# Performance work log

Measured on AMD Instinct MI355X. Metric: run time of the kernel, lower is better.

## Reference

```python
import jax, jax.numpy as jnp
import numpy as np

ALPHA = 0.2  # leaky relu negative slope
NEG_INF = -9e15


def setup_inputs() -> dict:
    key = jax.random.key(0)
    k1, k2, k3, k4, k5 = jax.random.split(key, 5)
    N, F_in, F_out, E = 4096, 64, 64, 8
    x = jax.random.normal(k1, (N, F_in), dtype=jnp.float32)
    adj = jax.random.randint(k2, (N, N), 0, 2, dtype=jnp.int32)
    edge_feats = jax.random.normal(k3, (N, N, E), dtype=jnp.float32)
    W = jax.random.normal(k4, (F_in, F_out), dtype=jnp.float32) * 0.1
    a = jax.random.normal(k5, (2 * F_out + E, 1), dtype=jnp.float32) * 0.1
    return {"x": x, "adj": adj, "edge_feats": edge_feats, "W": W, "a": a}


def reference(x, adj, edge_feats, W, a):
    F_out = W.shape[1]
    h = x @ W  # [N, F_out]
    # Original builds a_input[i,j] = concat(h_i, h_j, ef_ij) and dots with a.
    # Equivalent decomposition: e[i,j] = h_i.a1 + h_j.a2 + ef_ij.a3
    a1 = a[:F_out, 0]            # [F_out]
    a2 = a[F_out:2 * F_out, 0]   # [F_out]
    a3 = a[2 * F_out:, 0]        # [E]
    s1 = h @ a1                  # [N]
    s2 = h @ a2                  # [N]
    s3 = jnp.einsum('ije,e->ij', edge_feats, a3)  # [N, N]
    e = s1[:, None] + s2[None, :] + s3
    e = jnp.where(e > 0, e, ALPHA * e)  # leaky relu
    scores = jnp.where(adj > 0, e, NEG_INF)
    attention = jax.nn.softmax(scores, axis=1)
    # dropout p=0.0 (eval) -> identity
    h_prime = attention @ h  # [N, F_out]
    return jax.nn.elu(h_prime)  # concat=True
```

## Files before the change

kernel.cpp:

```cpp
#include <hip/hip_runtime.h>
#include <cstdint>
#include <cstddef>

#define LRELU_ALPHA 0.2f


typedef float f4 __attribute__((ext_vector_type(4)));

__device__ __forceinline__ f4 nt4(const float* p) {
    return __builtin_nontemporal_load((const f4*)p);
}

__global__ __launch_bounds__(256) void gat_prep(
    const float* __restrict__ x, const float* __restrict__ W,
    const float* __restrict__ a, float* __restrict__ h,
    float* __restrict__ s1, float* __restrict__ s2)
{
    __shared__ float Wl[64 * 64];
    const int tid = threadIdx.x;
    for (int idx = tid; idx < 64 * 64; idx += 256) Wl[idx] = W[idx];
    __syncthreads();

    const int wave = tid >> 6;
    const int lane = tid & 63;
    const int i = blockIdx.x * 4 + wave;

    const float xv = x[i * 64 + lane];
    float hv = 0.f;
#pragma unroll
    for (int k = 0; k < 64; ++k)
        hv = fmaf(__shfl(xv, k), Wl[k * 64 + lane], hv);
    h[i * 64 + lane] = hv;

    float v1 = hv * a[lane];
    float v2 = hv * a[64 + lane];
#pragma unroll
    for (int off = 32; off >= 1; off >>= 1) {
        v1 += __shfl_xor(v1, off);
        v2 += __shfl_xor(v2, off);
    }
    if (lane == 0) { s1[i] = v1; s2[i] = v2; }
}

__device__ __forceinline__ float bcast(float v, int l) {
    return __int_as_float(__builtin_amdgcn_readlane(__float_as_int(v), l));
}

__global__ __launch_bounds__(256, 4) void gat_attn(
    const float* __restrict__ ef, const int* __restrict__ adj,
    const float* __restrict__ a, const float* __restrict__ h,
    const float* __restrict__ s1, const float* __restrict__ s2,
    float* __restrict__ out)
{
    __shared__ float accs[4][4][64];
    __shared__ float lsums[4][4];

    const int tid  = threadIdx.x;
    const int w    = tid >> 6;
    const int lane = tid & 63;
    const int i0   = blockIdx.x * 4;

    float a3[8];
#pragma unroll
    for (int e = 0; e < 8; ++e) a3[e] = a[128 + e];

    float s1r[4];
#pragma unroll
    for (int r = 0; r < 4; ++r) s1r[r] = s1[i0 + r];

    float acc0 = 0.f, acc1 = 0.f, acc2 = 0.f, acc3 = 0.f;
    float ls0 = 0.f, ls1 = 0.f, ls2 = 0.f, ls3 = 0.f;

    const size_t efrow = (size_t)4096 * 8;

    int ad[4];
#pragma unroll
    for (int r = 0; r < 4; ++r)
        ad[r] = __builtin_nontemporal_load(adj + (size_t)(i0 + r) * 4096 + tid);

    for (int k = 0; k < 16; ++k) {
        const int j = tid + (k << 8);
        const float s2j = s2[j];

        int adn[4];
        if (k < 15) {
#pragma unroll
            for (int r = 0; r < 4; ++r)
                adn[r] = __builtin_nontemporal_load(
                    adj + (size_t)(i0 + r) * 4096 + j + 256);
        }

        float p0, p1, p2, p3;
        {
            float pv[4];
#pragma unroll
            for (int r = 0; r < 4; ++r) {
                float p = 0.f;
                if (ad[r] > 0) {
                    const float* efp = ef + (size_t)(i0 + r) * efrow + (size_t)j * 8;
                    const f4 e0 = nt4(efp);
                    const f4 e1 = nt4(efp + 4);
                    float s3 = e0.x * a3[0] + e0.y * a3[1] + e0.z * a3[2] + e0.w * a3[3]
                             + e1.x * a3[4] + e1.y * a3[5] + e1.z * a3[6] + e1.w * a3[7];
                    float e = s1r[r] + s2j + s3;
                    e = (e > 0.f) ? e : LRELU_ALPHA * e;
                    p = __expf(e);
                }
                pv[r] = p;
            }
            p0 = pv[0]; p1 = pv[1]; p2 = pv[2]; p3 = pv[3];
        }
        ls0 += p0; ls1 += p1; ls2 += p2; ls3 += p3;

        const int jw0 = (w << 6) + (k << 8);
        const float* __restrict__ hp = h + (size_t)jw0 * 64 + lane;
#pragma unroll 8
        for (int l = 0; l < 64; ++l) {
            const float hv = hp[l * 64];
            acc0 = fmaf(bcast(p0, l), hv, acc0);
            acc1 = fmaf(bcast(p1, l), hv, acc1);
            acc2 = fmaf(bcast(p2, l), hv, acc2);
            acc3 = fmaf(bcast(p3, l), hv, acc3);
        }

#pragma unroll
        for (int r = 0; r < 4; ++r) ad[r] = adn[r];
    }

#pragma unroll
    for (int off = 32; off >= 1; off >>= 1) {
        ls0 += __shfl_xor(ls0, off);
        ls1 += __shfl_xor(ls1, off);
        ls2 += __shfl_xor(ls2, off);
        ls3 += __shfl_xor(ls3, off);
    }
    if (lane == 0) {
        lsums[w][0] = ls0; lsums[w][1] = ls1;
        lsums[w][2] = ls2; lsums[w][3] = ls3;
    }
    accs[w][0][lane] = acc0;
    accs[w][1][lane] = acc1;
    accs[w][2][lane] = acc2;
    accs[w][3][lane] = acc3;
    __syncthreads();

    const float v = accs[0][w][lane] + accs[1][w][lane]
                  + accs[2][w][lane] + accs[3][w][lane];
    const float S = lsums[0][w] + lsums[1][w] + lsums[2][w] + lsums[3][w];
    float o = v / S;
    o = (o > 0.f) ? o : (__expf(o) - 1.f);
    out[(size_t)(i0 + w) * 64 + lane] = o;
}

extern "C" void kernel_launch(void* const* d_in, const int* in_sizes, int n_in,
                              void* d_out, int out_size, void* d_ws, size_t ws_size,
                              hipStream_t stream) {
    const float* x   = (const float*)d_in[0];
    const int*   adj = (const int*)  d_in[1];
    const float* ef  = (const float*)d_in[2];
    const float* W   = (const float*)d_in[3];
    const float* a   = (const float*)d_in[4];
    float* out = (float*)d_out;

    float* h  = (float*)d_ws;
    float* s1 = h + 4096 * 64;
    float* s2 = s1 + 4096;

    gat_prep<<<1024, 256, 0, stream>>>(x, W, a, h, s1, s2);
    gat_attn<<<1024, 256, 0, stream>>>(ef, adj, a, h, s1, s2, out);
}
```

Measured before the change: 759.7 us.

## Software-pipeline edge-feature and adjacency loads one and two iterations ahead

The attention kernel now prefetches the next iteration's edge-feature vectors into registers before the h-aggregation loop, and loads adjacency two iterations ahead. This hides the latency of the large streaming edge-feature reads behind the FMA loop. Scalar-uniform values (a3, s1) are also forced into scalar registers via readfirstlane. The cost is more live VGPRs, which may hurt occupancy under the 256x4 launch bound.

Result: no change. 761.8 us (+0.3%).

```diff
diff --git a/kernel.cpp b/kernel.cpp
--- a/kernel.cpp
+++ b/kernel.cpp
@@ -9,6 +9,10 @@
 
 __device__ __forceinline__ f4 nt4(const float* p) {
     return __builtin_nontemporal_load((const f4*)p);
+}
+
+__device__ __forceinline__ float sbcast(float v) {
+    return __int_as_float(__builtin_amdgcn_readfirstlane(__float_as_int(v)));
 }
 
 __global__ __launch_bounds__(256) void gat_prep(
@@ -62,34 +66,43 @@
 
     float a3[8];
 #pragma unroll
-    for (int e = 0; e < 8; ++e) a3[e] = a[128 + e];
+    for (int e = 0; e < 8; ++e) a3[e] = sbcast(a[128 + e]);
 
     float s1r[4];
 #pragma unroll
-    for (int r = 0; r < 4; ++r) s1r[r] = s1[i0 + r];
+    for (int r = 0; r < 4; ++r) s1r[r] = sbcast(s1[i0 + r]);
 
     float acc0 = 0.f, acc1 = 0.f, acc2 = 0.f, acc3 = 0.f;
     float ls0 = 0.f, ls1 = 0.f, ls2 = 0.f, ls3 = 0.f;
 
     const size_t efrow = (size_t)4096 * 8;
-
-    int ad[4];
+    const float* __restrict__ efr[4];
+#pragma unroll
+    for (int r = 0; r < 4; ++r) efr[r] = ef + (size_t)(i0 + r) * efrow;
+
+    int ad[4], adn[4];
 #pragma unroll
     for (int r = 0; r < 4; ++r)
         ad[r] = __builtin_nontemporal_load(adj + (size_t)(i0 + r) * 4096 + tid);
+
+    f4 ec0[4], ec1[4];
+#pragma unroll
+    for (int r = 0; r < 4; ++r) {
+        if (ad[r] > 0) {
+            const float* efp = efr[r] + (size_t)tid * 8;
+            ec0[r] = nt4(efp);
+            ec1[r] = nt4(efp + 4);
+        }
+    }
+#pragma unroll
+    for (int r = 0; r < 4; ++r)
+        adn[r] = __builtin_nontemporal_load(
+            adj + (size_t)(i0 + r) * 4096 + tid + 256);
 
     for (int k = 0; k < 16; ++k) {
         const int j = tid + (k << 8);
         const float s2j = s2[j];
 
-        int adn[4];
-        if (k < 15) {
-#pragma unroll
-            for (int r = 0; r < 4; ++r)
-                adn[r] = __builtin_nontemporal_load(
-                    adj + (size_t)(i0 + r) * 4096 + j + 256);
-        }
-
         float p0, p1, p2, p3;
         {
             float pv[4];
@@ -97,9 +110,8 @@
             for (int r = 0; r < 4; ++r) {
                 float p = 0.f;
                 if (ad[r] > 0) {
-                    const float* efp = ef + (size_t)(i0 + r) * efrow + (size_t)j * 8;
-                    const f4 e0 = nt4(efp);
-                    const f4 e1 = nt4(efp + 4);
+                    const f4 e0 = ec0[r];
+                    const f4 e1 = ec1[r];
                     float s3 = e0.x * a3[0] + e0.y * a3[1] + e0.z * a3[2] + e0.w * a3[3]
                              + e1.x * a3[4] + e1.y * a3[5] + e1.z * a3[6] + e1.w * a3[7];
                     float e = s1r[r] + s2j + s3;
@@ -112,6 +124,26 @@
         }
         ls0 += p0; ls1 += p1; ls2 += p2; ls3 += p3;
 
+        f4 en0[4], en1[4];
+        if (k < 15) {
+            const int jn = j + 256;
+#pragma unroll
+            for (int r = 0; r < 4; ++r) {
+                if (adn[r] > 0) {
+                    const float* efp = efr[r] + (size_t)jn * 8;
+                    en0[r] = nt4(efp);
+                    en1[r] = nt4(efp + 4);
+                }
+            }
+        }
+        int ad2[4];
+        if (k < 14) {
+#pragma unroll
+            for (int r = 0; r < 4; ++r)
+                ad2[r] = __builtin_nontemporal_load(
+                    adj + (size_t)(i0 + r) * 4096 + j + 512);
+        }
+
         const int jw0 = (w << 6) + (k << 8);
         const float* __restrict__ hp = h + (size_t)jw0 * 64 + lane;
 #pragma unroll 8
@@ -124,7 +156,12 @@
         }
 
 #pragma unroll
-        for (int r = 0; r < 4; ++r) ad[r] = adn[r];
+        for (int r = 0; r < 4; ++r) {
+            ad[r]  = adn[r];
+            adn[r] = ad2[r];
+            ec0[r] = en0[r];
+            ec1[r] = en1[r];
+        }
     }
 
 #pragma unroll
```

## Software-pipeline edge-feature and adjacency loads, stage s2 in LDS, register-buffer h

Applied to the files above, without the earlier changes.

Prefetches the next iteration's edge features unconditionally and the adjacency two iterations ahead, so global loads overlap the FMA loop. The adjacency mask becomes a select instead of a branch, s2 is staged in shared memory, and each 64-row h tile is loaded into registers before the broadcast-FMA loop. Scheduling barriers keep the prefetches ahead of the compute. The cost is that edge features are now read even where adjacency is zero, and the 64-float h buffer raises register pressure under the 4-blocks-per-CU launch bound.

After: 757.6 us. No clear change (-0.3%).

```diff
diff --git a/kernel.cpp b/kernel.cpp
--- a/kernel.cpp
+++ b/kernel.cpp
@@ -9,6 +9,14 @@
 
 __device__ __forceinline__ f4 nt4(const float* p) {
     return __builtin_nontemporal_load((const f4*)p);
+}
+
+__device__ __forceinline__ float sbcast(float v) {
+    return __int_as_float(__builtin_amdgcn_readfirstlane(__float_as_int(v)));
+}
+
+__device__ __forceinline__ float bcast(float v, int l) {
+    return __int_as_float(__builtin_amdgcn_readlane(__float_as_int(v), l));
 }
 
 __global__ __launch_bounds__(256) void gat_prep(
@@ -42,16 +50,13 @@
     if (lane == 0) { s1[i] = v1; s2[i] = v2; }
 }
 
-__device__ __forceinline__ float bcast(float v, int l) {
-    return __int_as_float(__builtin_amdgcn_readlane(__float_as_int(v), l));
-}
-
 __global__ __launch_bounds__(256, 4) void gat_attn(
     const float* __restrict__ ef, const int* __restrict__ adj,
     const float* __restrict__ a, const float* __restrict__ h,
     const float* __restrict__ s1, const float* __restrict__ s2,
     float* __restrict__ out)
 {
+    __shared__ float s2l[4096];
     __shared__ float accs[4][4][64];
     __shared__ float lsums[4][4];
 
@@ -60,63 +65,99 @@
     const int lane = tid & 63;
     const int i0   = blockIdx.x * 4;
 
+    for (int t = tid; t < 4096; t += 256) s2l[t] = s2[t];
+
     float a3[8];
 #pragma unroll
-    for (int e = 0; e < 8; ++e) a3[e] = a[128 + e];
-
+    for (int e = 0; e < 8; ++e) a3[e] = sbcast(a[128 + e]);
     float s1r[4];
 #pragma unroll
-    for (int r = 0; r < 4; ++r) s1r[r] = s1[i0 + r];
+    for (int r = 0; r < 4; ++r) s1r[r] = sbcast(s1[i0 + r]);
+
+    __syncthreads();
+
+    const size_t efrow = (size_t)4096 * 8;
+    const float* __restrict__ ef0 = ef + (size_t)(i0 + 0) * efrow;
+    const float* __restrict__ ef1 = ef + (size_t)(i0 + 1) * efrow;
+    const float* __restrict__ ef2 = ef + (size_t)(i0 + 2) * efrow;
+    const float* __restrict__ ef3 = ef + (size_t)(i0 + 3) * efrow;
+    const int* __restrict__ aj0 = adj + (size_t)(i0 + 0) * 4096;
+    const int* __restrict__ aj1 = adj + (size_t)(i0 + 1) * 4096;
+    const int* __restrict__ aj2 = adj + (size_t)(i0 + 2) * 4096;
+    const int* __restrict__ aj3 = adj + (size_t)(i0 + 3) * 4096;
 
     float acc0 = 0.f, acc1 = 0.f, acc2 = 0.f, acc3 = 0.f;
     float ls0 = 0.f, ls1 = 0.f, ls2 = 0.f, ls3 = 0.f;
 
-    const size_t efrow = (size_t)4096 * 8;
-
-    int ad[4];
-#pragma unroll
-    for (int r = 0; r < 4; ++r)
-        ad[r] = __builtin_nontemporal_load(adj + (size_t)(i0 + r) * 4096 + tid);
+    int ad[4], adn[4];
+    ad[0] = __builtin_nontemporal_load(aj0 + tid);
+    ad[1] = __builtin_nontemporal_load(aj1 + tid);
+    ad[2] = __builtin_nontemporal_load(aj2 + tid);
+    ad[3] = __builtin_nontemporal_load(aj3 + tid);
+    adn[0] = __builtin_nontemporal_load(aj0 + tid + 256);
+    adn[1] = __builtin_nontemporal_load(aj1 + tid + 256);
+    adn[2] = __builtin_nontemporal_load(aj2 + tid + 256);
+    adn[3] = __builtin_nontemporal_load(aj3 + tid + 256);
+
+    f4 ec0[4], ec1[4];
+    {
+        const size_t o = (size_t)tid * 8;
+        ec0[0] = nt4(ef0 + o); ec1[0] = nt4(ef0 + o + 4);
+        ec0[1] = nt4(ef1 + o); ec1[1] = nt4(ef1 + o + 4);
+        ec0[2] = nt4(ef2 + o); ec1[2] = nt4(ef2 + o + 4);
+        ec0[3] = nt4(ef3 + o); ec1[3] = nt4(ef3 + o + 4);
+    }
 
     for (int k = 0; k < 16; ++k) {
         const int j = tid + (k << 8);
-        const float s2j = s2[j];
-
-        int adn[4];
-        if (k < 15) {
-#pragma unroll
-            for (int r = 0; r < 4; ++r)
-                adn[r] = __builtin_nontemporal_load(
-                    adj + (size_t)(i0 + r) * 4096 + j + 256);
-        }
+        const float s2j = s2l[j];
 
         float p0, p1, p2, p3;
         {
             float pv[4];
 #pragma unroll
             for (int r = 0; r < 4; ++r) {
-                float p = 0.f;
-                if (ad[r] > 0) {
-                    const float* efp = ef + (size_t)(i0 + r) * efrow + (size_t)j * 8;
-                    const f4 e0 = nt4(efp);
-                    const f4 e1 = nt4(efp + 4);
-                    float s3 = e0.x * a3[0] + e0.y * a3[1] + e0.z * a3[2] + e0.w * a3[3]
-                             + e1.x * a3[4] + e1.y * a3[5] + e1.z * a3[6] + e1.w * a3[7];
-                    float e = s1r[r] + s2j + s3;
-                    e = (e > 0.f) ? e : LRELU_ALPHA * e;
-                    p = __expf(e);
-                }
-                pv[r] = p;
+                const f4 e0 = ec0[r];
+                const f4 e1 = ec1[r];
+                float s3 = e0.x * a3[0] + e0.y * a3[1] + e0.z * a3[2] + e0.w * a3[3]
+                         + e1.x * a3[4] + e1.y * a3[5] + e1.z * a3[6] + e1.w * a3[7];
+                float e = s1r[r] + s2j + s3;
+                e = (e > 0.f) ? e : LRELU_ALPHA * e;
+                pv[r] = (ad[r] > 0) ? __expf(e) : 0.f;
             }
             p0 = pv[0]; p1 = pv[1]; p2 = pv[2]; p3 = pv[3];
         }
         ls0 += p0; ls1 += p1; ls2 += p2; ls3 += p3;
 
-        const int jw0 = (w << 6) + (k << 8);
-        const float* __restrict__ hp = h + (size_t)jw0 * 64 + lane;
-#pragma unroll 8
+        float hreg[64];
+        const float* __restrict__ hp = h + (size_t)((w << 6) + (k << 8)) * 64 + lane;
+#pragma unroll
+        for (int l = 0; l < 64; ++l) hreg[l] = hp[l * 64];
+
+        __builtin_amdgcn_sched_barrier(0);
+
+        {
+            const int jn = (j + 256) & 4095;
+            const size_t o = (size_t)jn * 8;
+            ec0[0] = nt4(ef0 + o); ec1[0] = nt4(ef0 + o + 4);
+            ec0[1] = nt4(ef1 + o); ec1[1] = nt4(ef1 + o + 4);
+            ec0[2] = nt4(ef2 + o); ec1[2] = nt4(ef2 + o + 4);
+            ec0[3] = nt4(ef3 + o); ec1[3] = nt4(ef3 + o + 4);
+        }
+        int ad2[4];
+        {
+            const int j2 = (j + 512) & 4095;
+            ad2[0] = __builtin_nontemporal_load(aj0 + j2);
+            ad2[1] = __builtin_nontemporal_load(aj1 + j2);
+            ad2[2] = __builtin_nontemporal_load(aj2 + j2);
+            ad2[3] = __builtin_nontemporal_load(aj3 + j2);
+        }
+
+        __builtin_amdgcn_sched_barrier(0);
+
+#pragma unroll
         for (int l = 0; l < 64; ++l) {
-            const float hv = hp[l * 64];
+            const float hv = hreg[l];
             acc0 = fmaf(bcast(p0, l), hv, acc0);
             acc1 = fmaf(bcast(p1, l), hv, acc1);
             acc2 = fmaf(bcast(p2, l), hv, acc2);
@@ -124,7 +165,7 @@
         }
 
 #pragma unroll
-        for (int r = 0; r < 4; ++r) ad[r] = adn[r];
+        for (int r = 0; r < 4; ++r) { ad[r] = adn[r]; adn[r] = ad2[r]; }
     }
 
 #pragma unroll
```

## Process eight rows per block with 512 threads to halve h reloads

Applied to the files above, without the earlier changes.

Each attention block now handles 8 output rows instead of 4, using 512 threads and 8 waves, so every h tile read from global memory feeds twice as many accumulators. s2 is staged once per block in LDS, and a3/s1 are made wave-uniform with readfirstlane. The grid shrinks to 512 blocks, and register pressure per thread goes up with 8 accumulators and 8 prefetched adj values, which may reduce occupancy. The main cost is the ef stream (512MB), so the gain depends on whether h reloads or readlane work were limiting.

New measurement: 739.1 us. -2.7%, faster.

```diff
diff --git a/kernel.cpp b/kernel.cpp
--- a/kernel.cpp
+++ b/kernel.cpp
@@ -9,6 +9,14 @@
 
 __device__ __forceinline__ f4 nt4(const float* p) {
     return __builtin_nontemporal_load((const f4*)p);
+}
+
+__device__ __forceinline__ float sbcast(float v) {
+    return __int_as_float(__builtin_amdgcn_readfirstlane(__float_as_int(v)));
+}
+
+__device__ __forceinline__ float bcast(float v, int l) {
+    return __int_as_float(__builtin_amdgcn_readlane(__float_as_int(v), l));
 }
 
 __global__ __launch_bounds__(256) void gat_prep(
@@ -42,111 +50,106 @@
     if (lane == 0) { s1[i] = v1; s2[i] = v2; }
 }
 
-__device__ __forceinline__ float bcast(float v, int l) {
-    return __int_as_float(__builtin_amdgcn_readlane(__float_as_int(v), l));
-}
-
-__global__ __launch_bounds__(256, 4) void gat_attn(
+__global__ __launch_bounds__(512, 4) void gat_attn(
     const float* __restrict__ ef, const int* __restrict__ adj,
     const float* __restrict__ a, const float* __restrict__ h,
     const float* __restrict__ s1, const float* __restrict__ s2,
     float* __restrict__ out)
 {
-    __shared__ float accs[4][4][64];
-    __shared__ float lsums[4][4];
+    __shared__ float s2l[4096];
+    __shared__ float accs[8][8][64];
+    __shared__ float lsums[8][8];
 
     const int tid  = threadIdx.x;
     const int w    = tid >> 6;
     const int lane = tid & 63;
-    const int i0   = blockIdx.x * 4;
+    const int i0   = blockIdx.x * 8;
+
+    for (int t = tid; t < 4096; t += 512) s2l[t] = s2[t];
 
     float a3[8];
 #pragma unroll
-    for (int e = 0; e < 8; ++e) a3[e] = a[128 + e];
+    for (int e = 0; e < 8; ++e) a3[e] = sbcast(a[128 + e]);
+    float s1r[8];
+#pragma unroll
+    for (int r = 0; r < 8; ++r) s1r[r] = sbcast(s1[i0 + r]);
 
-    float s1r[4];
-#pragma unroll
-    for (int r = 0; r < 4; ++r) s1r[r] = s1[i0 + r];
-
-    float acc0 = 0.f, acc1 = 0.f, acc2 = 0.f, acc3 = 0.f;
-    float ls0 = 0.f, ls1 = 0.f, ls2 = 0.f, ls3 = 0.f;
+    __syncthreads();
 
     const size_t efrow = (size_t)4096 * 8;
 
-    int ad[4];
+    float acc[8], ls[8];
 #pragma unroll
-    for (int r = 0; r < 4; ++r)
+    for (int r = 0; r < 8; ++r) { acc[r] = 0.f; ls[r] = 0.f; }
+
+    int ad[8];
+#pragma unroll
+    for (int r = 0; r < 8; ++r)
         ad[r] = __builtin_nontemporal_load(adj + (size_t)(i0 + r) * 4096 + tid);
 
-    for (int k = 0; k < 16; ++k) {
-        const int j = tid + (k << 8);
-        const float s2j = s2[j];
+    for (int k = 0; k < 8; ++k) {
+        const int j = tid + (k << 9);
+        const float s2j = s2l[j];
 
-        int adn[4];
-        if (k < 15) {
+        int adn[8];
+        if (k < 7) {
 #pragma unroll
-            for (int r = 0; r < 4; ++r)
+            for (int r = 0; r < 8; ++r)
                 adn[r] = __builtin_nontemporal_load(
-                    adj + (size_t)(i0 + r) * 4096 + j + 256);
+                    adj + (size_t)(i0 + r) * 4096 + j + 512);
         }
 
-        float p0, p1, p2, p3;
-        {
-            float pv[4];
+        float p[8];
 #pragma unroll
-            for (int r = 0; r < 4; ++r) {
-                float p = 0.f;
-                if (ad[r] > 0) {
-                    const float* efp = ef + (size_t)(i0 + r) * efrow + (size_t)j * 8;
-                    const f4 e0 = nt4(efp);
-                    const f4 e1 = nt4(efp + 4);
-                    float s3 = e0.x * a3[0] + e0.y * a3[1] + e0.z * a3[2] + e0.w * a3[3]
-                             + e1.x * a3[4] + e1.y * a3[5] + e1.z * a3[6] + e1.w * a3[7];
-                    float e = s1r[r] + s2j + s3;
-                    e = (e > 0.f) ? e : LRELU_ALPHA * e;
-                    p = __expf(e);
-                }
-                pv[r] = p;
+        for (int r = 0; r < 8; ++r) {
+            float pp = 0.f;
+            if (ad[r] > 0) {
+                const float* efp = ef + (size_t)(i0 + r) * efrow + (size_t)j * 8;
+                const f4 e0 = nt4(efp);
+                const f4 e1 = nt4(efp + 4);
+                float s3 = e0.x * a3[0] + e0.y * a3[1] + e0.z * a3[2] + e0.w * a3[3]
+                         + e1.x * a3[4] + e1.y * a3[5] + e1.z * a3[6] + e1.w * a3[7];
+                float e = s1r[r] + s2j + s3;
+                e = (e > 0.f) ? e : LRELU_ALPHA * e;
+                pp = __expf(e);
             }
-            p0 = pv[0]; p1 = pv[1]; p2 = pv[2]; p3 = pv[3];
+            p[r] = pp;
+            ls[r] += pp;
         }
-        ls0 += p0; ls1 += p1; ls2 += p2; ls3 += p3;
 
-        const int jw0 = (w << 6) + (k << 8);
+        const int jw0 = (w << 6) + (k << 9);
         const float* __restrict__ hp = h + (size_t)jw0 * 64 + lane;
 #pragma unroll 8
         for (int l = 0; l < 64; ++l) {
             const float hv = hp[l * 64];
-            acc0 = fmaf(bcast(p0, l), hv, acc0);
-            acc1 = fmaf(bcast(p1, l), hv, acc1);
-            acc2 = fmaf(bcast(p2, l), hv, acc2);
-            acc3 = fmaf(bcast(p3, l), hv, acc3);
+#pragma unroll
+            for (int r = 0; r < 8; ++r)
+                acc[r] = fmaf(bcast(p[r], l), hv, acc[r]);
         }
 
 #pragma unroll
-        for (int r = 0; r < 4; ++r) ad[r] = adn[r];
+        for (int r = 0; r < 8; ++r) ad[r] = adn[r];
     }
 
 #pragma unroll
     for (int off = 32; off >= 1; off >>= 1) {
-        ls0 += __shfl_xor(ls0, off);
-        ls1 += __shfl_xor(ls1, off);
-        ls2 += __shfl_xor(ls2, off);
-        ls3 += __shfl_xor(ls3, off);
+#pragma unroll
+        for (int r = 0; r < 8; ++r) ls[r] += __shfl_xor(ls[r], off);
     }
     if (lane == 0) {
-        lsums[w][0] = ls0; lsums[w][1] = ls1;
-        lsums[w][2] = ls2; lsums[w][3] = ls3;
+#pragma unroll
+        for (int r = 0; r < 8; ++r) lsums[w][r] = ls[r];
     }
-    accs[w][0][lane] = acc0;
-    accs[w][1][lane] = acc1;
-    accs[w][2][lane] = acc2;
-    accs[w][3][lane] = acc3;
+#pragma unroll
+    for (int r = 0; r < 8; ++r) accs[w][r][lane] = acc[r];
     __syncthreads();
 
-    const float v = accs[0][w][lane] + accs[1][w][lane]
-                  + accs[2][w][lane] + accs[3][w][lane];
-    const float S = lsums[0][w] + lsums[1][w] + lsums[2][w] + lsums[3][w];
+    float v = 0.f, S = 0.f;
+#pragma unroll
+    for (int w2 = 0; w2 < 8; ++w2) {
+        v += accs[w2][w][lane];
+        S += lsums[w2][w];
+    }
     float o = v / S;
     o = (o > 0.f) ? o : (__expf(o) - 1.f);
     out[(size_t)(i0 + w) * 64 + lane] = o;
@@ -167,5 +170,5 @@
     float* s2 = s1 + 4096;
 
     gat_prep<<<1024, 256, 0, stream>>>(x, W, a, h, s1, s2);
-    gat_attn<<<1024, 256, 0, stream>>>(ef, adj, a, h, s1, s2, out);
+    gat_attn<<<512, 512, 0, stream>>>(ef, adj, a, h, s1, s2, out);
 }
```
